# Performance work log

Measured on AMD Instinct MI355X. Metric: run time of the kernel, lower is better.

Reference implementation:

```python
import jax, jax.numpy as jnp
import numpy as np

N_INPUT = 4096
N_NEURONS = 4096
T = 500
DT = 1.0
RATE = 0.05  # Bernoulli input spike probability per timestep

# LIF constants (Diehl&Cook-style excitatory / inhibitory populations)
E_REST, E_RESET, E_THRESH, E_TAU, E_REFRAC = -65.0, -65.0, -52.0, 100.0, 5.0
I_REST, I_RESET, I_THRESH, I_TAU, I_REFRAC = -60.0, -45.0, -40.0, 10.0, 2.0


def setup_inputs() -> dict:
    key = jax.random.key(0)
    k1, k2 = jax.random.split(key, 2)
    # Input group spike train: [T, n_input] of {0,1} floats (Poisson-like)
    inpts_X = (jax.random.uniform(k1, (T, N_INPUT)) < RATE).astype(jnp.float32)
    # X -> Ae learned weights (positive, small)
    w_xe = jax.random.uniform(k2, (N_INPUT, N_NEURONS), dtype=jnp.float32) * 0.3
    eye = jnp.eye(N_NEURONS, dtype=jnp.float32)
    # Ae -> Ai: one-to-one excitation; Ai -> Ae: all-but-self inhibition
    w_ei = 22.5 * eye
    w_ie = -17.5 * (1.0 - eye)
    return {"inpts_X": inpts_X, "w_xe": w_xe, "w_ei": w_ei, "w_ie": w_ie, "time": T}


def _lif(v, rc, inpt, rest, reset, thresh, tau, refrac):
    # Integrate only outside refractory period
    active = (rc <= 0).astype(v.dtype)
    v = v + (DT / tau) * (rest - v) + active * inpt
    rc = jnp.maximum(rc - DT, 0.0)
    s = (v >= thresh).astype(v.dtype)
    rc = jnp.where(s > 0, refrac, rc)
    v = jnp.where(s > 0, reset, v)
    return v, rc, s


def reference(inpts_X, w_xe, w_ei, w_ie, time):
    n_x = inpts_X.shape[1]
    n_e = w_xe.shape[1]
    n_i = w_ei.shape[1]
    f32 = inpts_X.dtype

    def step(carry, x_t):
        s_x, v_e, rc_e, s_e, v_i, rc_i, s_i = carry
        # get_inputs(): messages use spikes from the END of the previous step
        in_e = s_x @ w_xe + s_i @ w_ie   # inputs to excitatory group
        in_i = s_e @ w_ei                # inputs to inhibitory group
        s_x_new = x_t                    # InputGroup: s = current input row
        v_e2, rc_e2, s_e2 = _lif(v_e, rc_e, in_e, E_REST, E_RESET, E_THRESH, E_TAU, E_REFRAC)
        v_i2, rc_i2, s_i2 = _lif(v_i, rc_i, in_i, I_REST, I_RESET, I_THRESH, I_TAU, I_REFRAC)
        new_carry = (s_x_new, v_e2, rc_e2, s_e2, v_i2, rc_i2, s_i2)
        return new_carry, (s_x_new, s_e2, s_i2)

    init = (
        jnp.zeros((n_x,), f32),
        jnp.full((n_e,), E_REST, f32), jnp.zeros((n_e,), f32), jnp.zeros((n_e,), f32),
        jnp.full((n_i,), I_REST, f32), jnp.zeros((n_i,), f32), jnp.zeros((n_i,), f32),
    )
    _, (sx, se, si) = jax.lax.scan(step, init, inpts_X[: int(time)])
    # spikes dict -> concatenated [T, n_x + n_e + n_i]
    return jnp.concatenate([sx, se, si], axis=1)
```

## Files before the change

### kernel.cpp

```cpp
#include <hip/hip_runtime.h>

#define N 4096
#define OUTW 12288

__global__ void compact_spikes(const float* __restrict__ X, int* __restrict__ idx,
                               int* __restrict__ cnt, float* __restrict__ out, int T) {
    int t = blockIdx.x;
    const float* row = X + (size_t)t * N;
    __shared__ int counts[256];
    int tid = threadIdx.x;
    int base = tid * 16;
    float4 r0 = *(const float4*)(row + base);
    float4 r1 = *(const float4*)(row + base + 4);
    float4 r2 = *(const float4*)(row + base + 8);
    float4 r3 = *(const float4*)(row + base + 12);
    float* orow = out + (size_t)t * OUTW + base;
    *(float4*)(orow)      = r0;
    *(float4*)(orow + 4)  = r1;
    *(float4*)(orow + 8)  = r2;
    *(float4*)(orow + 12) = r3;
    float vals[16];
    *(float4*)(vals)      = r0;
    *(float4*)(vals + 4)  = r1;
    *(float4*)(vals + 8)  = r2;
    *(float4*)(vals + 12) = r3;
    int ks[16];
    int c = 0;
    #pragma unroll
    for (int q = 0; q < 16; ++q) {
        if (vals[q] != 0.0f) ks[c++] = base + q;
    }
    counts[tid] = c;
    __syncthreads();
    int off = 0;
    for (int i = 0; i < tid; ++i) off += counts[i];
    int* op = idx + (size_t)t * N;
    for (int q = 0; q < c; ++q) op[off + q] = ks[q];
    if (tid == 255) cnt[t] = off + c;
}

__global__ void gather_xw(const float* __restrict__ W, const int* __restrict__ idx,
                          const int* __restrict__ cnt, float* __restrict__ XW) {
    int b = blockIdx.x;
    int t = b >> 2;
    int tile = b & 3;
    int col = tile * 1024 + threadIdx.x * 4;
    float4 acc = {0.f, 0.f, 0.f, 0.f};
    if (t > 0) {
        int r = t - 1;
        int c = cnt[r];
        const int* ip = idx + (size_t)r * N;
        __shared__ int sidx[4096];
        for (int s = threadIdx.x; s < c; s += blockDim.x) sidx[s] = ip[s];
        __syncthreads();
        int s = 0;
        for (; s + 4 <= c; s += 4) {
            int k0 = sidx[s], k1 = sidx[s + 1], k2 = sidx[s + 2], k3 = sidx[s + 3];
            float4 w0 = *(const float4*)(W + (size_t)k0 * N + col);
            float4 w1 = *(const float4*)(W + (size_t)k1 * N + col);
            float4 w2 = *(const float4*)(W + (size_t)k2 * N + col);
            float4 w3 = *(const float4*)(W + (size_t)k3 * N + col);
            acc.x += w0.x; acc.y += w0.y; acc.z += w0.z; acc.w += w0.w;
            acc.x += w1.x; acc.y += w1.y; acc.z += w1.z; acc.w += w1.w;
            acc.x += w2.x; acc.y += w2.y; acc.z += w2.z; acc.w += w2.w;
            acc.x += w3.x; acc.y += w3.y; acc.z += w3.z; acc.w += w3.w;
        }
        for (; s < c; ++s) {
            int k = sidx[s];
            float4 w0 = *(const float4*)(W + (size_t)k * N + col);
            acc.x += w0.x; acc.y += w0.y; acc.z += w0.z; acc.w += w0.w;
        }
    }
    *(float4*)(XW + (size_t)t * N + col) = acc;
}

__global__ void __launch_bounds__(1024)
recurrent(const float* __restrict__ XW, unsigned char* __restrict__ pk, int T) {
    const int tid = threadIdx.x;
    const int lane = tid & 63;
    __shared__ unsigned int cS[3];
    if (tid < 3) cS[tid] = 0u;

    float ve[4], ref[4];
    unsigned int R = 0u;
    unsigned int E = 0u;
    unsigned int zp = 0u;
    unsigned char pw = 0;
    #pragma unroll
    for (int q = 0; q < 4; ++q) { ve[q] = -65.0f; ref[q] = 0.0f; }

    const float4* xwp = (const float4*)XW + tid;
    float4 xw = xwp[0];
    unsigned char* pkp = pk + tid;
    __syncthreads();

    int t = 0;
    #define STEP(PAR)                                                          \
    {                                                                          \
        unsigned int Sint = cS[(PAR + 2) % 3];     \
        if (t > 0) pkp[(size_t)(t - 1) * 1024] = pw;       \
        float4 xw_n = xw;                                                      \
        if (t + 1 < T) xw_n = xwp[(size_t)(t + 1) * 1024];                     \
        if (tid == 0) cS[(PAR + 1) % 3] = 0u;        \
          \
        unsigned int nz = (R | (R >> 1)) & 0x01010101u;                        \
        unsigned int z  = (nz ^ 0x01010101u) & E;                              \
        R = (R - nz) | (z << 1);                                               \
        int c0 = __popcll(__ballot((z & 0x000000ffu) != 0u));                  \
        int c1 = __popcll(__ballot((z & 0x0000ff00u) != 0u));                  \
        int c2 = __popcll(__ballot((z & 0x00ff0000u) != 0u));                  \
        int c3 = __popcll(__ballot((z & 0xff000000u) != 0u));                  \
        if (lane == 0) atomicAdd(&cS[PAR], (unsigned int)(c0 + c1 + c2 + c3)); \
                           \
        float Sf  = (float)Sint;                                               \
        float Sf1 = Sf - 1.0f;                              \
        const float xq[4] = {xw.x, xw.y, xw.z, xw.w};                          \
        unsigned int sbits = 0u;                                               \
        _Pragma("unroll")                                                      \
        for (int q = 0; q < 4; ++q) {                                          \
            unsigned int bq = (zp >> (q * 8)) & 1u;          \
            float dS = bq ? Sf1 : Sf;          \
            float in_e = xq[q] - 17.5f * dS;                \
            float in_sel = (ref[q] <= 0.0f) ? in_e : 0.0f;                     \
            float v = ve[q] + 0.01f * (-65.0f - ve[q]) + in_sel;               \
            float rc = fmaxf(ref[q] - 1.0f, 0.0f);                             \
            int s = (v >= -52.0f) ? 1 : 0;                                     \
            ref[q] = s ? 5.0f : rc;                                            \
            ve[q]  = s ? -65.0f : v;                                           \
            sbits |= (unsigned int)s << q;                                     \
        }                                                                      \
        E = (sbits * 0x00204081u) & 0x01010101u;        \
        unsigned int znib = (z * 0x10204080u) >> 24;    \
        pw = (unsigned char)(sbits | znib);                                    \
        zp = z;                                                                \
        xw = xw_n;                                                             \
        __syncthreads();                                                       \
        ++t;                                                                   \
    }

    for (int u = 0; u < 167; ++u) {
        STEP(0)
        STEP(1)
        STEP(2)
    }
    #undef STEP
}

__global__ void expand(const unsigned char* __restrict__ pk, float* __restrict__ out, int T) {
    int i = blockIdx.x * 256 + threadIdx.x;
    if (i >= T * 1024) return;
    int t = i >> 10;
    int g = i & 1023;
    unsigned int b = pk[i];
    float* orow = out + (size_t)t * OUTW + N + (size_t)g * 4;
    float4 se4 = {(float)(b & 1u), (float)((b >> 1) & 1u),
                  (float)((b >> 2) & 1u), (float)((b >> 3) & 1u)};
    float4 si4 = {(float)((b >> 4) & 1u), (float)((b >> 5) & 1u),
                  (float)((b >> 6) & 1u), (float)((b >> 7) & 1u)};
    *(float4*)orow = se4;
    *(float4*)(orow + N) = si4;
}

extern "C" void kernel_launch(void* const* d_in, const int* in_sizes, int n_in,
                              void* d_out, int out_size, void* d_ws, size_t ws_size,
                              hipStream_t stream) {
    const float* X   = (const float*)d_in[0];
    const float* Wxe = (const float*)d_in[1];
    int T = in_sizes[0] / N;
    float* out = (float*)d_out;

    float* XW = (float*)d_ws;
    int* idx  = (int*)((char*)d_ws + (size_t)T * N * 4);
    int* cnt  = (int*)((char*)d_ws + (size_t)2 * T * N * 4);
    unsigned char* pk = (unsigned char*)idx;

    compact_spikes<<<T, 256, 0, stream>>>(X, idx, cnt, out, T);
    gather_xw<<<T * 4, 256, 0, stream>>>(Wxe, idx, cnt, XW);
    recurrent<<<1, 1024, 0, stream>>>(XW, pk, T);
    expand<<<(T * 1024 + 255) / 256, 256, 0, stream>>>(pk, out, T);
}
```

Measured before the change: 467.8 us.

## Overlap input-weight gather with chunked recurrent LIF simulation in fused launches

Replaces the separate gather and single-block recurrent kernels with a sequence of fused launches over chunks of 100 timesteps. In each launch, block 0 advances the recurrent simulation over the previous chunk while the other blocks compute input-weight sums for the next chunk. Neuron state is saved to and restored from workspace between launches. The goal is to hide the gather cost behind the serial recurrence. The cost is extra launches, state round-trips, and fewer blocks working on the gather at once.

```diff
diff --git a/kernel.cpp b/kernel.cpp
--- a/kernel.cpp
+++ b/kernel.cpp
@@ -39,19 +39,105 @@
     if (tid == 255) cnt[t] = off + c;
 }
 
-__global__ void gather_xw(const float* __restrict__ W, const int* __restrict__ idx,
-                          const int* __restrict__ cnt, float* __restrict__ XW) {
-    int b = blockIdx.x;
-    int t = b >> 2;
-    int tile = b & 3;
-    int col = tile * 1024 + threadIdx.x * 4;
+__global__ void __launch_bounds__(1024)
+fused(const float* __restrict__ W, const int* __restrict__ idx,
+      const int* __restrict__ cnt, float* __restrict__ XW,
+      unsigned char* __restrict__ pk, float* __restrict__ state,
+      int ra, int rb, int ca, int cb, int T) {
+    __shared__ int sidx[4096];
+    __shared__ unsigned int cS[3];
+    const int tid = threadIdx.x;
+
+    if (blockIdx.x == 0) {
+        if (ca >= cb) return;
+        const int lane = tid & 63;
+        float ve[4], ref[4];
+        unsigned int R, E, zp;
+        unsigned char pw;
+        float* st = state + (size_t)tid * 12;
+        if (ca == 0) {
+            #pragma unroll
+            for (int q = 0; q < 4; ++q) { ve[q] = -65.0f; ref[q] = 0.0f; }
+            R = 0u; E = 0u; zp = 0u; pw = 0;
+            if (tid == 0) { cS[0] = 0u; cS[1] = 0u; cS[2] = 0u; }
+        } else {
+            float4 a = *(float4*)(st);
+            float4 b = *(float4*)(st + 4);
+            uint4  c = *(uint4*)(st + 8);
+            ve[0] = a.x; ve[1] = a.y; ve[2] = a.z; ve[3] = a.w;
+            ref[0] = b.x; ref[1] = b.y; ref[2] = b.z; ref[3] = b.w;
+            R = c.x; E = c.y; zp = c.z; pw = (unsigned char)c.w;
+            if (tid == 0) {
+                cS[0] = 0u; cS[1] = 0u;
+                cS[2] = *(unsigned int*)(state + 12 * 1024);
+            }
+        }
+        const float4* xwp = (const float4*)XW + tid;
+        float4 xw = xwp[(size_t)ca * 1024];
+        unsigned char* pkp = pk + tid;
+        int prev = 2, cur = 0, nxt = 1;
+        __syncthreads();
+
+        for (int t = ca; t < cb; ++t) {
+            unsigned int Sint = cS[prev];
+            if (t > 0) pkp[(size_t)(t - 1) * 1024] = pw;
+            float4 xw_n = xw;
+            if (t + 1 < cb) xw_n = xwp[(size_t)(t + 1) * 1024];
+            if (tid == 0) cS[nxt] = 0u;
+            unsigned int nz = (R | (R >> 1)) & 0x01010101u;
+            unsigned int z  = (nz ^ 0x01010101u) & E;
+            R = (R - nz) | (z << 1);
+            int c0 = __popcll(__ballot((z & 0x000000ffu) != 0u));
+            int c1 = __popcll(__ballot((z & 0x0000ff00u) != 0u));
+            int c2 = __popcll(__ballot((z & 0x00ff0000u) != 0u));
+            int c3 = __popcll(__ballot((z & 0xff000000u) != 0u));
+            if (lane == 0) atomicAdd(&cS[cur], (unsigned int)(c0 + c1 + c2 + c3));
+            float Sf  = (float)Sint;
+            float Sf1 = Sf - 1.0f;
+            const float xq[4] = {xw.x, xw.y, xw.z, xw.w};
+            unsigned int sbits = 0u;
+            #pragma unroll
+            for (int q = 0; q < 4; ++q) {
+                unsigned int bq = (zp >> (q * 8)) & 1u;
+                float dS = bq ? Sf1 : Sf;
+                float in_e = xq[q] - 17.5f * dS;
+                float in_sel = (ref[q] <= 0.0f) ? in_e : 0.0f;
+                float v = ve[q] + 0.01f * (-65.0f - ve[q]) + in_sel;
+                float rc = fmaxf(ref[q] - 1.0f, 0.0f);
+                int s = (v >= -52.0f) ? 1 : 0;
+                ref[q] = s ? 5.0f : rc;
+                ve[q]  = s ? -65.0f : v;
+                sbits |= (unsigned int)s << q;
+            }
+            E = (sbits * 0x00204081u) & 0x01010101u;
+            unsigned int znib = (z * 0x10204080u) >> 24;
+            pw = (unsigned char)(sbits | znib);
+            zp = z;
+            xw = xw_n;
+            int tmp = prev; prev = cur; cur = nxt; nxt = tmp;
+            __syncthreads();
+        }
+        pkp[(size_t)(cb - 1) * 1024] = pw;
+        if (cb < T) {
+            float4 a = {ve[0], ve[1], ve[2], ve[3]};
+            float4 b = {ref[0], ref[1], ref[2], ref[3]};
+            uint4  c = {R, E, zp, (unsigned int)pw};
+            *(float4*)(st)     = a;
+            *(float4*)(st + 4) = b;
+            *(uint4*)(st + 8)  = c;
+            if (tid == 0) *(unsigned int*)(state + 12 * 1024) = cS[prev];
+        }
+        return;
+    }
+
+    int r = ra + (int)blockIdx.x - 1;
+    if (r >= rb) return;
+    int col = tid * 4;
     float4 acc = {0.f, 0.f, 0.f, 0.f};
-    if (t > 0) {
-        int r = t - 1;
-        int c = cnt[r];
-        const int* ip = idx + (size_t)r * N;
-        __shared__ int sidx[4096];
-        for (int s = threadIdx.x; s < c; s += blockDim.x) sidx[s] = ip[s];
+    if (r > 0) {
+        int c = cnt[r - 1];
+        const int* ip = idx + (size_t)(r - 1) * N;
+        for (int s = tid; s < c; s += 1024) sidx[s] = ip[s];
         __syncthreads();
         int s = 0;
         for (; s + 4 <= c; s += 4) {
@@ -71,79 +157,7 @@
             acc.x += w0.x; acc.y += w0.y; acc.z += w0.z; acc.w += w0.w;
         }
     }
-    *(float4*)(XW + (size_t)t * N + col) = acc;
-}
-
-__global__ void __launch_bounds__(1024)
-recurrent(const float* __restrict__ XW, unsigned char* __restrict__ pk, int T) {
-    const int tid = threadIdx.x;
-    const int lane = tid & 63;
-    __shared__ unsigned int cS[3];
-    if (tid < 3) cS[tid] = 0u;
-
-    float ve[4], ref[4];
-    unsigned int R = 0u;
-    unsigned int E = 0u;
-    unsigned int zp = 0u;
-    unsigned char pw = 0;
-    #pragma unroll
-    for (int q = 0; q < 4; ++q) { ve[q] = -65.0f; ref[q] = 0.0f; }
-
-    const float4* xwp = (const float4*)XW + tid;
-    float4 xw = xwp[0];
-    unsigned char* pkp = pk + tid;
-    __syncthreads();
-
-    int t = 0;
-    #define STEP(PAR)                                                          \
-    {                                                                          \
-        unsigned int Sint = cS[(PAR + 2) % 3];     \
-        if (t > 0) pkp[(size_t)(t - 1) * 1024] = pw;       \
-        float4 xw_n = xw;                                                      \
-        if (t + 1 < T) xw_n = xwp[(size_t)(t + 1) * 1024];                     \
-        if (tid == 0) cS[(PAR + 1) % 3] = 0u;        \
-          \
-        unsigned int nz = (R | (R >> 1)) & 0x01010101u;                        \
-        unsigned int z  = (nz ^ 0x01010101u) & E;                              \
-        R = (R - nz) | (z << 1);                                               \
-        int c0 = __popcll(__ballot((z & 0x000000ffu) != 0u));                  \
-        int c1 = __popcll(__ballot((z & 0x0000ff00u) != 0u));                  \
-        int c2 = __popcll(__ballot((z & 0x00ff0000u) != 0u));                  \
-        int c3 = __popcll(__ballot((z & 0xff000000u) != 0u));                  \
-        if (lane == 0) atomicAdd(&cS[PAR], (unsigned int)(c0 + c1 + c2 + c3)); \
-                           \
-        float Sf  = (float)Sint;                                               \
-        float Sf1 = Sf - 1.0f;                              \
-        const float xq[4] = {xw.x, xw.y, xw.z, xw.w};                          \
-        unsigned int sbits = 0u;                                               \
-        _Pragma("unroll")                                                      \
-        for (int q = 0; q < 4; ++q) {                                          \
-            unsigned int bq = (zp >> (q * 8)) & 1u;          \
-            float dS = bq ? Sf1 : Sf;          \
-            float in_e = xq[q] - 17.5f * dS;                \
-            float in_sel = (ref[q] <= 0.0f) ? in_e : 0.0f;                     \
-            float v = ve[q] + 0.01f * (-65.0f - ve[q]) + in_sel;               \
-            float rc = fmaxf(ref[q] - 1.0f, 0.0f);                             \
-            int s = (v >= -52.0f) ? 1 : 0;                                     \
-            ref[q] = s ? 5.0f : rc;                                            \
-            ve[q]  = s ? -65.0f : v;                                           \
-            sbits |= (unsigned int)s << q;                                     \
-        }                                                                      \
-        E = (sbits * 0x00204081u) & 0x01010101u;        \
-        unsigned int znib = (z * 0x10204080u) >> 24;    \
-        pw = (unsigned char)(sbits | znib);                                    \
-        zp = z;                                                                \
-        xw = xw_n;                                                             \
-        __syncthreads();                                                       \
-        ++t;                                                                   \
-    }
-
-    for (int u = 0; u < 167; ++u) {
-        STEP(0)
-        STEP(1)
-        STEP(2)
-    }
-    #undef STEP
+    *(float4*)(XW + (size_t)r * N + col) = acc;
 }
 
 __global__ void expand(const unsigned char* __restrict__ pk, float* __restrict__ out, int T) {
@@ -173,9 +187,24 @@
     int* idx  = (int*)((char*)d_ws + (size_t)T * N * 4);
     int* cnt  = (int*)((char*)d_ws + (size_t)2 * T * N * 4);
     unsigned char* pk = (unsigned char*)idx;
+    float* state = (float*)((char*)idx + 40 * 16384);
 
     compact_spikes<<<T, 256, 0, stream>>>(X, idx, cnt, out, T);
-    gather_xw<<<T * 4, 256, 0, stream>>>(Wxe, idx, cnt, XW);
-    recurrent<<<1, 1024, 0, stream>>>(XW, pk, T);
+
+    const int C = 100;
+    int nch = (T + C - 1) / C;
+    for (int i = 0; i <= nch; ++i) {
+        int ra = i * C, rb = (i + 1) * C;
+        if (ra > T) ra = T;
+        if (rb > T) rb = T;
+        int ca = (i - 1) * C, cb = i * C;
+        if (ca < 0) ca = 0;
+        if (cb > T) cb = T;
+        if (i == 0) { ca = cb = 0; }
+        int grid = 1 + (rb - ra);
+        fused<<<grid, 1024, 0, stream>>>(Wxe, idx, cnt, XW, pk, state,
+                                         ra, rb, ca, cb, T);
+    }
+
     expand<<<(T * 1024 + 255) / 256, 256, 0, stream>>>(pk, out, T);
 }
```

Result: slower. 480.0 us (+2.6%).
